# Optimization experiments

Hardware: AMD Instinct MI355X
Metric: run time of the kernel (lower is better)

## Reference

```python
import jax, jax.numpy as jnp
import numpy as np

B, T, D_IN, H, D_OUT, MLP_H = 512, 1024, 64, 256, 64, 256


def setup_inputs() -> dict:
    key = jax.random.key(0)
    ks = jax.random.split(key, 12)
    s_ih = 1.0 / np.sqrt(H)
    return {
        "x": jax.random.normal(ks[0], (B, T, D_IN), dtype=jnp.float32),
        "mask": jax.random.uniform(ks[1], (B, T, 1), dtype=jnp.float32),
        "h0": jax.random.normal(ks[2], (B, H), dtype=jnp.float32),
        "c0": jax.random.normal(ks[3], (B, H), dtype=jnp.float32),
        # LSTMCell params (PyTorch layout: gates in i, f, g, o order)
        "W_ih": jax.random.uniform(ks[4], (4 * H, D_IN), minval=-s_ih, maxval=s_ih, dtype=jnp.float32),
        "W_hh": jax.random.uniform(ks[5], (4 * H, H), minval=-s_ih, maxval=s_ih, dtype=jnp.float32),
        "b_ih": jax.random.uniform(ks[6], (4 * H,), minval=-s_ih, maxval=s_ih, dtype=jnp.float32),
        "b_hh": jax.random.uniform(ks[7], (4 * H,), minval=-s_ih, maxval=s_ih, dtype=jnp.float32),
        # output MLP: Linear(H, MLP_H) -> ReLU -> Linear(MLP_H, D_OUT)
        "W1": jax.random.normal(ks[8], (MLP_H, H), dtype=jnp.float32) * (1.0 / np.sqrt(H)),
        "b1": jnp.zeros((MLP_H,), dtype=jnp.float32),
        "W2": jax.random.normal(ks[9], (D_OUT, MLP_H), dtype=jnp.float32) * (1.0 / np.sqrt(MLP_H)),
        "b2": jnp.zeros((D_OUT,), dtype=jnp.float32),
    }


def _lstm_scan(x, h0, c0, W_ih, W_hh, b_ih, b_hh):
    # precompute input projections for all timesteps: [T, B, 4H]
    x_tb = jnp.swapaxes(x, 0, 1)  # [T, B, D_IN]
    x_proj = jnp.einsum("tbd,gd->tbg", x_tb, W_ih) + b_ih + b_hh

    def step(carry, xp):
        h, c = carry
        gates = xp + h @ W_hh.T  # [B, 4H]
        i, f, g, o = jnp.split(gates, 4, axis=-1)
        i = jax.nn.sigmoid(i)
        f = jax.nn.sigmoid(f)
        g = jnp.tanh(g)
        o = jax.nn.sigmoid(o)
        c = f * c + i * g
        h = o * jnp.tanh(c)
        return (h, c), h

    _, hs = jax.lax.scan(step, (h0, c0), x_proj)  # hs: [T, B, H]
    return jnp.swapaxes(hs, 0, 1)  # [B, T, H]


def reference(x, mask, h0, c0, W_ih, W_hh, b_ih, b_hh, W1, b1, W2, b2):
    hs = _lstm_scan(x, h0, c0, W_ih, W_hh, b_ih, b_hh)  # [B, T, H]
    y = jax.nn.relu(hs @ W1.T + b1) @ W2.T + b2  # [B, T, D_OUT]
    return y * mask
```

## Files before the change

### kernel.cpp

```cpp
#include <hip/hip_runtime.h>
#include <stdint.h>
#include <stddef.h>

#define T_STEPS 1024
#define BATCH   512
#define HID     256
#define DIN     64

typedef __attribute__((ext_vector_type(8))) short short8;
typedef __attribute__((ext_vector_type(4))) short short4v;
typedef __attribute__((ext_vector_type(2))) short short2v;
typedef __attribute__((ext_vector_type(4))) float float4v;

static __device__ __forceinline__ short f2bf(float f) {
  union { float f; unsigned u; } v; v.f = f;
  unsigned r = (v.u + 0x7FFFu + ((v.u >> 16) & 1u)) >> 16;
  return (short)r;
}
static __device__ __forceinline__ float sigm(float x) {
  return 1.0f / (1.0f + __expf(-x));
}
static __device__ __forceinline__ float tanh_f(float x) {
  return 2.0f / (1.0f + __expf(-2.0f * x)) - 1.0f;
}

__global__ __launch_bounds__(512, 2) void lstm_kernel(
    const float* __restrict__ x, const float* __restrict__ h0,
    const float* __restrict__ c0, const float* __restrict__ W_ih,
    const float* __restrict__ W_hh, const float* __restrict__ b_ih,
    const float* __restrict__ b_hh, float* __restrict__ exch,
    uint16_t* __restrict__ hs) {
  const int tid   = threadIdx.x;
  const int blk   = blockIdx.x;
  const int group = blk & 31;
  const int half  = blk >> 5;
  const int b0    = group * 16;
  const int w     = tid >> 6;
  const int lane  = tid & 63;
  const int quad  = lane >> 4;
  const int l16   = lane & 15;
  const int partner = blk ^ 32;

  __shared__ short Alds[16 * 328];
  __shared__ float Glds[16 * 516];

  short8 bw[10][4];
#pragma unroll
  for (int j = 0; j < 10; ++j) {
    int ktA = (j < 4) ? (half * 4 + j) : (j < 8) ? ((1 - half) * 4 + (j - 4)) : j;
#pragma unroll
    for (int nt = 0; nt < 4; ++nt) {
      int n_loc = w * 64 + nt * 16 + l16;
      int gate  = n_loc >> 7;
      int hh    = n_loc & 127;
      int grow  = gate * 256 + half * 128 + hh;
      const float* src = (ktA < 8)
          ? (W_hh + (size_t)grow * 256 + ktA * 32 + quad * 8)
          : (W_ih + (size_t)grow * 64 + (ktA - 8) * 32 + quad * 8);
      short8 bv;
#pragma unroll
      for (int e = 0; e < 8; ++e) bv[e] = f2bf(src[e]);
      bw[j][nt] = bv;
    }
  }

  const int urow = tid >> 5;
  const int hh0  = (tid & 31) * 4;
  const int xc   = (tid & 31) * 2;
  float bias[4][4];
  float c_reg[4];
#pragma unroll
  for (int g = 0; g < 4; ++g) {
    const float* bi = b_ih + g * 256 + half * 128 + hh0;
    const float* bh = b_hh + g * 256 + half * 128 + hh0;
#pragma unroll
    for (int r = 0; r < 4; ++r) bias[g][r] = bi[r] + bh[r];
  }
  {
    const float* c0p = c0 + (size_t)(b0 + urow) * 256 + half * 128 + hh0;
#pragma unroll
    for (int r = 0; r < 4; ++r) c_reg[r] = c0p[r];
  }

  const int widx = urow * 64 + (hh0 >> 1);
  unsigned long long* sbuf[2];
  const unsigned long long* pbuf[2];
#pragma unroll
  for (int bfi = 0; bfi < 2; ++bfi) {
    sbuf[bfi] = (unsigned long long*)(exch + ((size_t)blk * 2 + bfi) * 2048) + widx;
    pbuf[bfi] = (const unsigned long long*)(exch + ((size_t)partner * 2 + bfi) * 2048) + widx;
  }

  {
    int c8 = (tid & 31) * 8;
    const float* hp = h0 + (size_t)(b0 + urow) * 256 + c8;
    short8 hv;
#pragma unroll
    for (int e = 0; e < 8; ++e) hv[e] = f2bf(hp[e]);
    *(short8*)&Alds[urow * 328 + c8] = hv;
    const float* xp = x + ((size_t)(b0 + urow) * T_STEPS + 0) * DIN + xc;
    short2v xv2; xv2[0] = f2bf(xp[0]); xv2[1] = f2bf(xp[1]);
    *(short2v*)&Alds[urow * 328 + 256 + xc] = xv2;
  }
  __syncthreads();

  const int ownbase = half * 128;
  const int pbase   = (1 - half) * 128;

  for (int t = 0; t < T_STEPS; ++t) {
    float4v acc[4] = {{0.f,0.f,0.f,0.f},{0.f,0.f,0.f,0.f},
                      {0.f,0.f,0.f,0.f},{0.f,0.f,0.f,0.f}};
    int tn = (t + 1 < T_STEPS) ? (t + 1) : t;
    const float* xp = x + ((size_t)(b0 + urow) * T_STEPS + tn) * DIN + xc;
    float xa = xp[0], xb = xp[1];

#pragma unroll
    for (int j = 0; j < 4; ++j) {
      short8 a = *(const short8*)&Alds[l16 * 328 + ownbase + j * 32 + quad * 8];
#pragma unroll
      for (int nt = 0; nt < 4; ++nt)
        acc[nt] = __builtin_amdgcn_mfma_f32_16x16x32_bf16(a, bw[j][nt], acc[nt], 0, 0, 0);
    }
#pragma unroll
    for (int j = 8; j < 10; ++j) {
      short8 a = *(const short8*)&Alds[l16 * 328 + 256 + (j - 8) * 32 + quad * 8];
#pragma unroll
      for (int nt = 0; nt < 4; ++nt)
        acc[nt] = __builtin_amdgcn_mfma_f32_16x16x32_bf16(a, bw[j][nt], acc[nt], 0, 0, 0);
    }

    if (t > 0) {
      int buf = (t - 1) & 1;
      unsigned tag = 1u ^ (((unsigned)(t - 1) >> 1) & 1u);
      const unsigned long long* p = pbuf[buf];
      unsigned long long w0, w1;
      int guard = 0;
      for (;;) {
        w0 = __hip_atomic_load(p,     __ATOMIC_RELAXED, __HIP_MEMORY_SCOPE_AGENT);
        w1 = __hip_atomic_load(p + 1, __ATOMIC_RELAXED, __HIP_MEMORY_SCOPE_AGENT);
        bool ok = (((unsigned)w0 & 1u) == tag) & ((((unsigned)(w0 >> 32)) & 1u) == tag) &
                  (((unsigned)w1 & 1u) == tag) & ((((unsigned)(w1 >> 32)) & 1u) == tag);
        if (ok) break;
        if (++guard > 4096) break;
      }
      union { unsigned u; float f; } f0, f1, f2, f3;
      f0.u = (unsigned)w0; f1.u = (unsigned)(w0 >> 32);
      f2.u = (unsigned)w1; f3.u = (unsigned)(w1 >> 32);
      short4v pv4;
      pv4[0] = f2bf(f0.f); pv4[1] = f2bf(f1.f);
      pv4[2] = f2bf(f2.f); pv4[3] = f2bf(f3.f);
      *(short4v*)&Alds[urow * 328 + pbase + hh0] = pv4;
    }
    __syncthreads();

#pragma unroll
    for (int j = 4; j < 8; ++j) {
      short8 a = *(const short8*)&Alds[l16 * 328 + pbase + (j - 4) * 32 + quad * 8];
#pragma unroll
      for (int nt = 0; nt < 4; ++nt)
        acc[nt] = __builtin_amdgcn_mfma_f32_16x16x32_bf16(a, bw[j][nt], acc[nt], 0, 0, 0);
    }
#pragma unroll
    for (int nt = 0; nt < 4; ++nt) {
      int col = w * 64 + nt * 16 + l16;
#pragma unroll
      for (int r = 0; r < 4; ++r)
        Glds[(quad * 4 + r) * 516 + col] = acc[nt][r];
    }
    __syncthreads();

    float4v ip = *(const float4v*)&Glds[urow * 516 + 0   + hh0];
    float4v fp = *(const float4v*)&Glds[urow * 516 + 128 + hh0];
    float4v gp = *(const float4v*)&Glds[urow * 516 + 256 + hh0];
    float4v op = *(const float4v*)&Glds[urow * 516 + 384 + hh0];
    float hf[4];
    short hb[4];
#pragma unroll
    for (int r = 0; r < 4; ++r) {
      float iv = sigm(ip[r] + bias[0][r]);
      float fv = sigm(fp[r] + bias[1][r]);
      float gv = tanh_f(gp[r] + bias[2][r]);
      float ov = sigm(op[r] + bias[3][r]);
      float cv = fv * c_reg[r] + iv * gv;
      c_reg[r] = cv;
      hf[r] = ov * tanh_f(cv);
      hb[r] = f2bf(hf[r]);
    }
    {
      int buf = t & 1;
      unsigned tag = 1u ^ (((unsigned)t >> 1) & 1u);
      union { float f; unsigned u; } u0, u1, u2, u3;
      u0.f = hf[0]; u1.f = hf[1]; u2.f = hf[2]; u3.f = hf[3];
      unsigned long long w0 = (unsigned long long)((u0.u & ~1u) | tag)
                            | ((unsigned long long)((u1.u & ~1u) | tag) << 32);
      unsigned long long w1 = (unsigned long long)((u2.u & ~1u) | tag)
                            | ((unsigned long long)((u3.u & ~1u) | tag) << 32);
      __hip_atomic_store(sbuf[buf],     w0, __ATOMIC_RELAXED, __HIP_MEMORY_SCOPE_AGENT);
      __hip_atomic_store(sbuf[buf] + 1, w1, __ATOMIC_RELAXED, __HIP_MEMORY_SCOPE_AGENT);
    }
    short4v hv4; hv4[0] = hb[0]; hv4[1] = hb[1]; hv4[2] = hb[2]; hv4[3] = hb[3];
    *(short4v*)&Alds[urow * 328 + ownbase + hh0] = hv4;
    *(short4v*)(hs + ((size_t)(b0 + urow) * T_STEPS + t) * HID + ownbase + hh0) = hv4;
    short2v xv2; xv2[0] = f2bf(xa); xv2[1] = f2bf(xb);
    *(short2v*)&Alds[urow * 328 + 256 + xc] = xv2;
    __syncthreads();
  }
}

__global__ void prep_kernel(const float* __restrict__ W1, const float* __restrict__ W2,
                            short* __restrict__ W1b, short* __restrict__ W2b) {
  int i = blockIdx.x * 512 + threadIdx.x;
  if (i < 65536) W1b[i] = f2bf(W1[i]);
  else           W2b[i - 65536] = f2bf(W2[i - 65536]);
}

__global__ __launch_bounds__(512, 2) void mlp_kernel(
    const uint16_t* __restrict__ hs, const short* __restrict__ W1b,
    const float* __restrict__ b1, const short* __restrict__ W2b,
    const float* __restrict__ b2, const float* __restrict__ mask,
    float* __restrict__ y) {
  const int tid   = threadIdx.x;
  const int rows0 = blockIdx.x * 128;
  const int w     = tid >> 6;
  const int lane  = tid & 63;
  const int quad  = lane >> 4;
  const int l16   = lane & 15;

  __shared__ short S[128 * 264];

#pragma unroll
  for (int kk = 0; kk < 8; ++kk) {
    int c   = tid + kk * 512;
    int row = c >> 5;
    int off = (c & 31) * 8;
    *(short8*)&S[row * 264 + off] =
        *(const short8*)(hs + (size_t)(rows0 + row) * HID + off);
  }

  short8 bf1[2][8];
  float  b1v[2];
#pragma unroll
  for (int nt = 0; nt < 2; ++nt) {
    int n = w * 32 + nt * 16 + l16;
    b1v[nt] = b1[n];
#pragma unroll
    for (int kt = 0; kt < 8; ++kt)
      bf1[nt][kt] = *(const short8*)(W1b + (size_t)n * 256 + kt * 32 + quad * 8);
  }
  __syncthreads();

  float4v acc1[2][8];
#pragma unroll
  for (int nt = 0; nt < 2; ++nt)
#pragma unroll
    for (int mt = 0; mt < 8; ++mt) acc1[nt][mt] = (float4v){0.f,0.f,0.f,0.f};
#pragma unroll
  for (int kt = 0; kt < 8; ++kt) {
#pragma unroll
    for (int mt = 0; mt < 8; ++mt) {
      short8 a = *(const short8*)&S[(mt * 16 + l16) * 264 + kt * 32 + quad * 8];
#pragma unroll
      for (int nt = 0; nt < 2; ++nt)
        acc1[nt][mt] = __builtin_amdgcn_mfma_f32_16x16x32_bf16(a, bf1[nt][kt], acc1[nt][mt], 0, 0, 0);
    }
  }
  __syncthreads();

#pragma unroll
  for (int nt = 0; nt < 2; ++nt) {
    int col = w * 32 + nt * 16 + l16;
#pragma unroll
    for (int mt = 0; mt < 8; ++mt)
#pragma unroll
      for (int r = 0; r < 4; ++r) {
        float v = acc1[nt][mt][r] + b1v[nt];
        v = v > 0.f ? v : 0.f;
        S[(mt * 16 + quad * 4 + r) * 264 + col] = f2bf(v);
      }
  }
  __syncthreads();

  const int mt2 = w >> 1;
  short8 a2[8];
#pragma unroll
  for (int kt = 0; kt < 8; ++kt)
    a2[kt] = *(const short8*)(W2b + (size_t)(mt2 * 16 + l16) * 256 + kt * 32 + quad * 8);
  float4v acc2[4] = {{0.f,0.f,0.f,0.f},{0.f,0.f,0.f,0.f},
                     {0.f,0.f,0.f,0.f},{0.f,0.f,0.f,0.f}};
#pragma unroll
  for (int kt = 0; kt < 8; ++kt) {
#pragma unroll
    for (int nt2 = 0; nt2 < 4; ++nt2) {
      int n0 = (w & 1) * 64 + nt2 * 16;
      short8 b = *(const short8*)&S[(n0 + l16) * 264 + kt * 32 + quad * 8];
      acc2[nt2] = __builtin_amdgcn_mfma_f32_16x16x32_bf16(a2[kt], b, acc2[nt2], 0, 0, 0);
    }
  }
  const float* b2p = b2 + mt2 * 16 + quad * 4;
  float b2v0 = b2p[0], b2v1 = b2p[1], b2v2 = b2p[2], b2v3 = b2p[3];
#pragma unroll
  for (int nt2 = 0; nt2 < 4; ++nt2) {
    int R = rows0 + (w & 1) * 64 + nt2 * 16 + l16;
    float m = mask[R];
    float4v out;
    out[0] = (acc2[nt2][0] + b2v0) * m;
    out[1] = (acc2[nt2][1] + b2v1) * m;
    out[2] = (acc2[nt2][2] + b2v2) * m;
    out[3] = (acc2[nt2][3] + b2v3) * m;
    *(float4v*)(y + (size_t)R * 64 + mt2 * 16 + quad * 4) = out;
  }
}

extern "C" void kernel_launch(void* const* d_in, const int* in_sizes, int n_in,
                              void* d_out, int out_size, void* d_ws, size_t ws_size,
                              hipStream_t stream) {
  (void)in_sizes; (void)n_in; (void)out_size; (void)ws_size;
  const float* x    = (const float*)d_in[0];
  const float* mask = (const float*)d_in[1];
  const float* h0   = (const float*)d_in[2];
  const float* c0   = (const float*)d_in[3];
  const float* W_ih = (const float*)d_in[4];
  const float* W_hh = (const float*)d_in[5];
  const float* b_ih = (const float*)d_in[6];
  const float* b_hh = (const float*)d_in[7];
  const float* W1   = (const float*)d_in[8];
  const float* b1   = (const float*)d_in[9];
  const float* W2   = (const float*)d_in[10];
  const float* b2   = (const float*)d_in[11];
  float* y = (float*)d_out;

  char* ws = (char*)d_ws;
  float*    exch = (float*)ws;
  short*    W1b  = (short*)(ws + (1u << 20));
  short*    W2b  = (short*)(ws + (1u << 20) + 131072);
  uint16_t* hs   = (uint16_t*)(ws + (2u << 20));

  prep_kernel<<<160, 512, 0, stream>>>(W1, W2, W1b, W2b);
  lstm_kernel<<<64, 512, 0, stream>>>(x, h0, c0, W_ih, W_hh, b_ih, b_hh, exch, hs);
  mlp_kernel<<<4096, 512, 0, stream>>>(hs, W1b, b1, W2b, b2, mask, y);
}
```

Before: 3.668 ms.

## Add same-XCD fast path for partner hidden-state exchange via sc0 16-byte messages

Each block records its XCC id in a table and checks whether its partner block runs on the same XCD. If it does, the per-step hidden-state exchange uses a single 16-byte sc0 store and load carrying bf16 payload between step-id sentinels. This is meant to poll at L2 rather than device scope, cutting the latency of the serial cross-block handoff at every timestep. The original tagged fp32 exchange is still written every step and serves as the fallback, so store traffic rises and correctness depends on a 16-byte store being seen atomically.

```diff
diff --git a/kernel.cpp b/kernel.cpp
--- a/kernel.cpp
+++ b/kernel.cpp
@@ -11,6 +11,7 @@
 typedef __attribute__((ext_vector_type(4))) short short4v;
 typedef __attribute__((ext_vector_type(2))) short short2v;
 typedef __attribute__((ext_vector_type(4))) float float4v;
+typedef __attribute__((ext_vector_type(4))) unsigned int uint4v;
 
 static __device__ __forceinline__ short f2bf(float f) {
   union { float f; unsigned u; } v; v.f = f;
@@ -22,6 +23,16 @@
 }
 static __device__ __forceinline__ float tanh_f(float x) {
   return 2.0f / (1.0f + __expf(-2.0f * x)) - 1.0f;
+}
+
+static __device__ __forceinline__ void st16_sc0(float* p, uint4v v) {
+  asm volatile("global_store_dwordx4 %0, %1, off sc0" :: "v"(p), "v"(v) : "memory");
+}
+static __device__ __forceinline__ uint4v ld16_sc0(const float* p) {
+  uint4v r;
+  asm volatile("global_load_dwordx4 %0, %1, off sc0\n\ts_waitcnt vmcnt(0)"
+               : "=v"(r) : "v"(p) : "memory");
+  return r;
 }
 
 __global__ __launch_bounds__(512, 2) void lstm_kernel(
@@ -29,6 +40,7 @@
     const float* __restrict__ c0, const float* __restrict__ W_ih,
     const float* __restrict__ W_hh, const float* __restrict__ b_ih,
     const float* __restrict__ b_hh, float* __restrict__ exch,
+    float* __restrict__ exchf, unsigned* __restrict__ tbl,
     uint16_t* __restrict__ hs) {
   const int tid   = threadIdx.x;
   const int blk   = blockIdx.x;
@@ -43,6 +55,45 @@
 
   __shared__ short Alds[16 * 328];
   __shared__ float Glds[16 * 516];
+  __shared__ int s_fastex;
+
+  const int urow = tid >> 5;
+  const int hh0  = (tid & 31) * 4;
+  const int xc   = (tid & 31) * 2;
+
+  const int widx = urow * 64 + (hh0 >> 1);
+  unsigned long long* sbuf[2];
+  const unsigned long long* pbuf[2];
+  float* sfast[2];
+  const float* pfast[2];
+#pragma unroll
+  for (int bfi = 0; bfi < 2; ++bfi) {
+    sbuf[bfi]  = (unsigned long long*)(exch + ((size_t)blk * 2 + bfi) * 2048) + widx;
+    pbuf[bfi]  = (const unsigned long long*)(exch + ((size_t)partner * 2 + bfi) * 2048) + widx;
+    sfast[bfi] = exchf + ((size_t)blk * 2 + bfi) * 2048 + (widx << 1);
+    pfast[bfi] = exchf + ((size_t)partner * 2 + bfi) * 2048 + (widx << 1);
+  }
+
+  {
+    uint4v z; z[0] = 0u; z[1] = 0u; z[2] = 0u; z[3] = 0u;
+    st16_sc0(sfast[0], z);
+    st16_sc0(sfast[1], z);
+  }
+  __syncthreads();
+  if (tid == 0) {
+    int xcd;
+    asm volatile("s_getreg_b32 %0, hwreg(HW_REG_XCC_ID)" : "=s"(xcd));
+    unsigned my = 0x5AB00000u | ((unsigned)xcd & 0xFFu);
+    __hip_atomic_store(&tbl[blk], my, __ATOMIC_RELAXED, __HIP_MEMORY_SCOPE_AGENT);
+    unsigned pv = 0;
+    for (int g2 = 0; g2 < (1 << 16); ++g2) {
+      pv = __hip_atomic_load(&tbl[partner], __ATOMIC_RELAXED, __HIP_MEMORY_SCOPE_AGENT);
+      if ((pv & 0xFFFFFF00u) == 0x5AB00000u) break;
+      __builtin_amdgcn_s_sleep(8);
+    }
+    s_fastex = (((pv & 0xFFFFFF00u) == 0x5AB00000u) &&
+                ((pv & 0xFFu) == (my & 0xFFu))) ? 1 : 0;
+  }
 
   short8 bw[10][4];
 #pragma unroll
@@ -64,9 +115,6 @@
     }
   }
 
-  const int urow = tid >> 5;
-  const int hh0  = (tid & 31) * 4;
-  const int xc   = (tid & 31) * 2;
   float bias[4][4];
   float c_reg[4];
 #pragma unroll
@@ -80,15 +128,6 @@
     const float* c0p = c0 + (size_t)(b0 + urow) * 256 + half * 128 + hh0;
 #pragma unroll
     for (int r = 0; r < 4; ++r) c_reg[r] = c0p[r];
-  }
-
-  const int widx = urow * 64 + (hh0 >> 1);
-  unsigned long long* sbuf[2];
-  const unsigned long long* pbuf[2];
-#pragma unroll
-  for (int bfi = 0; bfi < 2; ++bfi) {
-    sbuf[bfi] = (unsigned long long*)(exch + ((size_t)blk * 2 + bfi) * 2048) + widx;
-    pbuf[bfi] = (const unsigned long long*)(exch + ((size_t)partner * 2 + bfi) * 2048) + widx;
   }
 
   {
@@ -103,6 +142,7 @@
     *(short2v*)&Alds[urow * 328 + 256 + xc] = xv2;
   }
   __syncthreads();
+  const int fastex = s_fastex;
 
   const int ownbase = half * 128;
   const int pbase   = (1 - half) * 128;
@@ -131,24 +171,39 @@
 
     if (t > 0) {
       int buf = (t - 1) & 1;
-      unsigned tag = 1u ^ (((unsigned)(t - 1) >> 1) & 1u);
-      const unsigned long long* p = pbuf[buf];
-      unsigned long long w0, w1;
-      int guard = 0;
-      for (;;) {
-        w0 = __hip_atomic_load(p,     __ATOMIC_RELAXED, __HIP_MEMORY_SCOPE_AGENT);
-        w1 = __hip_atomic_load(p + 1, __ATOMIC_RELAXED, __HIP_MEMORY_SCOPE_AGENT);
-        bool ok = (((unsigned)w0 & 1u) == tag) & ((((unsigned)(w0 >> 32)) & 1u) == tag) &
-                  (((unsigned)w1 & 1u) == tag) & ((((unsigned)(w1 >> 32)) & 1u) == tag);
-        if (ok) break;
-        if (++guard > 4096) break;
+      short4v pv4;
+      bool got = false;
+      if (fastex) {
+        unsigned expect = 0xC0DE0000u + (unsigned)(t - 1);
+        for (int g2 = 0; g2 < 128; ++g2) {
+          uint4v v = ld16_sc0(pfast[buf]);
+          if (v[0] == expect && v[3] == expect) {
+            pv4[0] = (short)(v[1] & 0xFFFFu); pv4[1] = (short)(v[1] >> 16);
+            pv4[2] = (short)(v[2] & 0xFFFFu); pv4[3] = (short)(v[2] >> 16);
+            got = true;
+            break;
+          }
+        }
       }
-      union { unsigned u; float f; } f0, f1, f2, f3;
-      f0.u = (unsigned)w0; f1.u = (unsigned)(w0 >> 32);
-      f2.u = (unsigned)w1; f3.u = (unsigned)(w1 >> 32);
-      short4v pv4;
-      pv4[0] = f2bf(f0.f); pv4[1] = f2bf(f1.f);
-      pv4[2] = f2bf(f2.f); pv4[3] = f2bf(f3.f);
+      if (!got) {
+        unsigned tag = 1u ^ (((unsigned)(t - 1) >> 1) & 1u);
+        const unsigned long long* p = pbuf[buf];
+        unsigned long long w0, w1;
+        int guard = 0;
+        for (;;) {
+          w0 = __hip_atomic_load(p,     __ATOMIC_RELAXED, __HIP_MEMORY_SCOPE_AGENT);
+          w1 = __hip_atomic_load(p + 1, __ATOMIC_RELAXED, __HIP_MEMORY_SCOPE_AGENT);
+          bool ok = (((unsigned)w0 & 1u) == tag) & ((((unsigned)(w0 >> 32)) & 1u) == tag) &
+                    (((unsigned)w1 & 1u) == tag) & ((((unsigned)(w1 >> 32)) & 1u) == tag);
+          if (ok) break;
+          if (++guard > 4096) break;
+        }
+        union { unsigned u; float f; } g0, g1, g2, g3;
+        g0.u = (unsigned)w0; g1.u = (unsigned)(w0 >> 32);
+        g2.u = (unsigned)w1; g3.u = (unsigned)(w1 >> 32);
+        pv4[0] = f2bf(g0.f); pv4[1] = f2bf(g1.f);
+        pv4[2] = f2bf(g2.f); pv4[3] = f2bf(g3.f);
+      }
       *(short4v*)&Alds[urow * 328 + pbase + hh0] = pv4;
     }
     __syncthreads();
@@ -188,6 +243,15 @@
     }
     {
       int buf = t & 1;
+      if (fastex) {
+        unsigned idw = 0xC0DE0000u + (unsigned)t;
+        unsigned pay01 = (unsigned)(unsigned short)hb[0]
+                       | ((unsigned)(unsigned short)hb[1] << 16);
+        unsigned pay23 = (unsigned)(unsigned short)hb[2]
+                       | ((unsigned)(unsigned short)hb[3] << 16);
+        uint4v sv; sv[0] = idw; sv[1] = pay01; sv[2] = pay23; sv[3] = idw;
+        st16_sc0(sfast[buf], sv);
+      }
       unsigned tag = 1u ^ (((unsigned)t >> 1) & 1u);
       union { float f; unsigned u; } u0, u1, u2, u3;
       u0.f = hf[0]; u1.f = hf[1]; u2.f = hf[2]; u3.f = hf[3];
@@ -208,8 +272,11 @@
 }
 
 __global__ void prep_kernel(const float* __restrict__ W1, const float* __restrict__ W2,
-                            short* __restrict__ W1b, short* __restrict__ W2b) {
+                            short* __restrict__ W1b, short* __restrict__ W2b,
+                            unsigned* __restrict__ tbl) {
   int i = blockIdx.x * 512 + threadIdx.x;
+  if (i < 64)
+    __hip_atomic_store(&tbl[i], 0u, __ATOMIC_RELAXED, __HIP_MEMORY_SCOPE_AGENT);
   if (i < 65536) W1b[i] = f2bf(W1[i]);
   else           W2b[i - 65536] = f2bf(W2[i - 65536]);
 }
@@ -330,12 +397,14 @@
   float* y = (float*)d_out;
 
   char* ws = (char*)d_ws;
-  float*    exch = (float*)ws;
-  short*    W1b  = (short*)(ws + (1u << 20));
-  short*    W2b  = (short*)(ws + (1u << 20) + 131072);
-  uint16_t* hs   = (uint16_t*)(ws + (2u << 20));
-
-  prep_kernel<<<160, 512, 0, stream>>>(W1, W2, W1b, W2b);
-  lstm_kernel<<<64, 512, 0, stream>>>(x, h0, c0, W_ih, W_hh, b_ih, b_hh, exch, hs);
+  float*    exch  = (float*)ws;
+  float*    exchf = (float*)(ws + (1u << 20));
+  short*    W1b   = (short*)(ws + (2u << 20));
+  short*    W2b   = (short*)(ws + (2u << 20) + 131072);
+  unsigned* tbl   = (unsigned*)(ws + (2u << 20) + 131072 + 32768);
+  uint16_t* hs    = (uint16_t*)(ws + (3u << 20));
+
+  prep_kernel<<<160, 512, 0, stream>>>(W1, W2, W1b, W2b, tbl);
+  lstm_kernel<<<64, 512, 0, stream>>>(x, h0, c0, W_ih, W_hh, b_ih, b_hh, exch, exchf, tbl, hs);
   mlp_kernel<<<4096, 512, 0, stream>>>(hs, W1b, b1, W2b, b2, mask, y);
 }
```

Measured after the change: 7.724 ms. +110.6%, slower.

## Interleave two batch groups per block to hide partner h-exchange latency

Applied to the files above, without the earlier changes.

Each LSTM block now processes two 16-row batch groups (A and B) using 32 blocks instead of 64. The partner h-exchange for one group overlaps the MFMA work of the other. The gate layout is reorganized so each lane holds all four gates for its hidden unit, which removes the Glds staging buffer and one barrier. Polling now uses non-blocking atomic_add-0 issued early with s_sleep backoff, and the hs global store is deferred by one step. The trade-off is half the blocks and CUs in use, more registers, and more serial work per block.

```diff
diff --git a/kernel.cpp b/kernel.cpp
--- a/kernel.cpp
+++ b/kernel.cpp
@@ -22,6 +22,21 @@
 }
 static __device__ __forceinline__ float tanh_f(float x) {
   return 2.0f / (1.0f + __expf(-2.0f * x)) - 1.0f;
+}
+
+static __device__ __forceinline__ void apoll_issue(const unsigned long long* p,
+                                                   unsigned long long& r0,
+                                                   unsigned long long& r1) {
+  unsigned long long z = 0;
+  asm volatile("global_atomic_add_x2 %0, %2, %3, off sc0\n\t"
+               "global_atomic_add_x2 %1, %2, %3, off offset:8 sc0"
+               : "=&v"(r0), "=&v"(r1)
+               : "v"(p), "v"(z)
+               : "memory");
+}
+static __device__ __forceinline__ void apoll_wait(unsigned long long& r0,
+                                                  unsigned long long& r1) {
+  asm volatile("s_waitcnt vmcnt(0)" : "+v"(r0), "+v"(r1) :: "memory");
 }
 
 __global__ __launch_bounds__(512, 2) void lstm_kernel(
@@ -32,179 +47,251 @@
     uint16_t* __restrict__ hs) {
   const int tid   = threadIdx.x;
   const int blk   = blockIdx.x;
-  const int group = blk & 31;
-  const int half  = blk >> 5;
-  const int b0    = group * 16;
+  const int p     = blk & 15;
+  const int half  = blk >> 4;
+  const int partner = blk ^ 16;
+  const int b0A   = (2 * p) * 16;
+  const int b0B   = (2 * p + 1) * 16;
   const int w     = tid >> 6;
   const int lane  = tid & 63;
   const int quad  = lane >> 4;
   const int l16   = lane & 15;
-  const int partner = blk ^ 32;
-
-  __shared__ short Alds[16 * 328];
-  __shared__ float Glds[16 * 516];
+  const int w16l  = w * 16 + l16;
+
+  __shared__ short AldsA[16 * 328];
+  __shared__ short AldsB[16 * 328];
+
+  const int urow = tid >> 5;
+  const int hh0  = (tid & 31) * 4;
+  const int xc   = (tid & 31) * 2;
+
+  const int widx = tid * 2;
+  unsigned long long* const sb_base =
+      (unsigned long long*)exch + (size_t)blk * 4096 + widx;
+  const unsigned long long* const pb_base =
+      (const unsigned long long*)exch + (size_t)partner * 4096 + widx;
 
   short8 bw[10][4];
 #pragma unroll
   for (int j = 0; j < 10; ++j) {
     int ktA = (j < 4) ? (half * 4 + j) : (j < 8) ? ((1 - half) * 4 + (j - 4)) : j;
 #pragma unroll
-    for (int nt = 0; nt < 4; ++nt) {
-      int n_loc = w * 64 + nt * 16 + l16;
-      int gate  = n_loc >> 7;
-      int hh    = n_loc & 127;
-      int grow  = gate * 256 + half * 128 + hh;
+    for (int g = 0; g < 4; ++g) {
+      int grow = g * 256 + half * 128 + w16l;
       const float* src = (ktA < 8)
           ? (W_hh + (size_t)grow * 256 + ktA * 32 + quad * 8)
           : (W_ih + (size_t)grow * 64 + (ktA - 8) * 32 + quad * 8);
       short8 bv;
 #pragma unroll
       for (int e = 0; e < 8; ++e) bv[e] = f2bf(src[e]);
-      bw[j][nt] = bv;
-    }
-  }
-
-  const int urow = tid >> 5;
-  const int hh0  = (tid & 31) * 4;
-  const int xc   = (tid & 31) * 2;
-  float bias[4][4];
-  float c_reg[4];
-#pragma unroll
-  for (int g = 0; g < 4; ++g) {
-    const float* bi = b_ih + g * 256 + half * 128 + hh0;
-    const float* bh = b_hh + g * 256 + half * 128 + hh0;
-#pragma unroll
-    for (int r = 0; r < 4; ++r) bias[g][r] = bi[r] + bh[r];
-  }
-  {
-    const float* c0p = c0 + (size_t)(b0 + urow) * 256 + half * 128 + hh0;
-#pragma unroll
-    for (int r = 0; r < 4; ++r) c_reg[r] = c0p[r];
-  }
-
-  const int widx = urow * 64 + (hh0 >> 1);
-  unsigned long long* sbuf[2];
-  const unsigned long long* pbuf[2];
-#pragma unroll
-  for (int bfi = 0; bfi < 2; ++bfi) {
-    sbuf[bfi] = (unsigned long long*)(exch + ((size_t)blk * 2 + bfi) * 2048) + widx;
-    pbuf[bfi] = (const unsigned long long*)(exch + ((size_t)partner * 2 + bfi) * 2048) + widx;
+      bw[j][g] = bv;
+    }
+  }
+
+  const int hh_abs = half * 128 + w16l;
+  float bias_g[4];
+#pragma unroll
+  for (int g = 0; g < 4; ++g)
+    bias_g[g] = b_ih[g * 256 + hh_abs] + b_hh[g * 256 + hh_abs];
+  float cA[4], cB[4];
+#pragma unroll
+  for (int r = 0; r < 4; ++r) {
+    cA[r] = c0[(size_t)(b0A + quad * 4 + r) * 256 + hh_abs];
+    cB[r] = c0[(size_t)(b0B + quad * 4 + r) * 256 + hh_abs];
   }
 
   {
     int c8 = (tid & 31) * 8;
-    const float* hp = h0 + (size_t)(b0 + urow) * 256 + c8;
     short8 hv;
-#pragma unroll
-    for (int e = 0; e < 8; ++e) hv[e] = f2bf(hp[e]);
-    *(short8*)&Alds[urow * 328 + c8] = hv;
-    const float* xp = x + ((size_t)(b0 + urow) * T_STEPS + 0) * DIN + xc;
-    short2v xv2; xv2[0] = f2bf(xp[0]); xv2[1] = f2bf(xp[1]);
-    *(short2v*)&Alds[urow * 328 + 256 + xc] = xv2;
+    const float* hpA = h0 + (size_t)(b0A + urow) * 256 + c8;
+#pragma unroll
+    for (int e = 0; e < 8; ++e) hv[e] = f2bf(hpA[e]);
+    *(short8*)&AldsA[urow * 328 + c8] = hv;
+    const float* hpB = h0 + (size_t)(b0B + urow) * 256 + c8;
+#pragma unroll
+    for (int e = 0; e < 8; ++e) hv[e] = f2bf(hpB[e]);
+    *(short8*)&AldsB[urow * 328 + c8] = hv;
+    const float* xpA = x + ((size_t)(b0A + urow) * T_STEPS + 0) * DIN + xc;
+    short2v xv; xv[0] = f2bf(xpA[0]); xv[1] = f2bf(xpA[1]);
+    *(short2v*)&AldsA[urow * 328 + 256 + xc] = xv;
+    const float* xpB = x + ((size_t)(b0B + urow) * T_STEPS + 0) * DIN + xc;
+    xv[0] = f2bf(xpB[0]); xv[1] = f2bf(xpB[1]);
+    *(short2v*)&AldsB[urow * 328 + 256 + xc] = xv;
   }
   __syncthreads();
 
   const int ownbase = half * 128;
   const int pbase   = (1 - half) * 128;
 
+#define PH1(AL, ACC)                                                          \
+  _Pragma("unroll")                                                           \
+  for (int j = 0; j < 4; ++j) {                                               \
+    short8 a = *(const short8*)&AL[l16 * 328 + ownbase + j * 32 + quad * 8];  \
+    _Pragma("unroll")                                                         \
+    for (int g = 0; g < 4; ++g)                                               \
+      ACC[g] = __builtin_amdgcn_mfma_f32_16x16x32_bf16(a, bw[j][g], ACC[g], 0, 0, 0); \
+  }                                                                           \
+  _Pragma("unroll")                                                           \
+  for (int j = 8; j < 10; ++j) {                                              \
+    short8 a = *(const short8*)&AL[l16 * 328 + 256 + (j - 8) * 32 + quad * 8];\
+    _Pragma("unroll")                                                         \
+    for (int g = 0; g < 4; ++g)                                               \
+      ACC[g] = __builtin_amdgcn_mfma_f32_16x16x32_bf16(a, bw[j][g], ACC[g], 0, 0, 0); \
+  }
+
+#define PH2(AL, ACC)                                                          \
+  _Pragma("unroll")                                                           \
+  for (int j = 4; j < 8; ++j) {                                               \
+    short8 a = *(const short8*)&AL[l16 * 328 + pbase + (j - 4) * 32 + quad * 8]; \
+    _Pragma("unroll")                                                         \
+    for (int g = 0; g < 4; ++g)                                               \
+      ACC[g] = __builtin_amdgcn_mfma_f32_16x16x32_bf16(a, bw[j][g], ACC[g], 0, 0, 0); \
+  }
+
+#define CHECK_POLL(PB, R0, R1, PV)                                            \
+  do {                                                                        \
+    unsigned tag2 = (((unsigned)(t - 1) >> 1) & 1u) ? 3u : 1u;                \
+    int guard = 0;                                                            \
+    for (;;) {                                                                \
+      bool ok = ((((unsigned)R0) & 3u) == tag2) &                             \
+                ((((unsigned)(R0 >> 32)) & 3u) == tag2) &                     \
+                ((((unsigned)R1) & 3u) == tag2) &                             \
+                ((((unsigned)(R1 >> 32)) & 3u) == tag2);                      \
+      if (ok) break;                                                          \
+      if (++guard > 4096) break;                                              \
+      __builtin_amdgcn_s_sleep(1);                                            \
+      apoll_issue(PB, R0, R1);                                                \
+      apoll_wait(R0, R1);                                                     \
+    }                                                                         \
+    union { unsigned u; float f; } q0, q1, q2, q3;                            \
+    q0.u = (unsigned)R0; q1.u = (unsigned)(R0 >> 32);                         \
+    q2.u = (unsigned)R1; q3.u = (unsigned)(R1 >> 32);                         \
+    PV[0] = f2bf(q0.f); PV[1] = f2bf(q1.f);                                   \
+    PV[2] = f2bf(q2.f); PV[3] = f2bf(q3.f);                                   \
+  } while (0)
+
+#define UPD(ACC, CREG, HF, HB)                                                \
+  _Pragma("unroll")                                                           \
+  for (int r = 0; r < 4; ++r) {                                               \
+    float iv = sigm(ACC[0][r] + bias_g[0]);                                   \
+    float fv = sigm(ACC[1][r] + bias_g[1]);                                   \
+    float gv = tanh_f(ACC[2][r] + bias_g[2]);                                 \
+    float ov = sigm(ACC[3][r] + bias_g[3]);                                   \
+    float cv = fv * CREG[r] + iv * gv;                                        \
+    CREG[r] = cv;                                                             \
+    HF[r] = ov * tanh_f(cv);                                                  \
+    HB[r] = f2bf(HF[r]);                                                      \
+  }
+
+#define PUB(SB, HF)                                                           \
+  do {                                                                        \
+    unsigned tag2 = (((unsigned)t >> 1) & 1u) ? 3u : 1u;                      \
+    union { float f; unsigned u; } u0, u1, u2, u3;                            \
+    u0.f = HF[0]; u1.f = HF[1]; u2.f = HF[2]; u3.f = HF[3];                   \
+    unsigned long long w0 = (unsigned long long)((u0.u & ~3u) | tag2)         \
+                          | ((unsigned long long)((u1.u & ~3u) | tag2) << 32);\
+    unsigned long long w1 = (unsigned long long)((u2.u & ~3u) | tag2)         \
+                          | ((unsigned long long)((u3.u & ~3u) | tag2) << 32);\
+    __hip_atomic_store(SB,     w0, __ATOMIC_RELAXED, __HIP_MEMORY_SCOPE_AGENT); \
+    __hip_atomic_store(SB + 1, w1, __ATOMIC_RELAXED, __HIP_MEMORY_SCOPE_AGENT); \
+  } while (0)
+
   for (int t = 0; t < T_STEPS; ++t) {
-    float4v acc[4] = {{0.f,0.f,0.f,0.f},{0.f,0.f,0.f,0.f},
-                      {0.f,0.f,0.f,0.f},{0.f,0.f,0.f,0.f}};
+    const unsigned long long* pbA = pb_base + (size_t)(((t - 1) & 1)) * 1024;
+    const unsigned long long* pbB = pb_base + (size_t)(2 + ((t - 1) & 1)) * 1024;
+    unsigned long long* sbA = sb_base + (size_t)(t & 1) * 1024;
+    unsigned long long* sbB = sb_base + (size_t)(2 + (t & 1)) * 1024;
+
+    unsigned long long rA0 = 0, rA1 = 0, rB0 = 0, rB1 = 0;
+    float4v accA[4] = {{0.f,0.f,0.f,0.f},{0.f,0.f,0.f,0.f},
+                       {0.f,0.f,0.f,0.f},{0.f,0.f,0.f,0.f}};
+    float4v accB[4] = {{0.f,0.f,0.f,0.f},{0.f,0.f,0.f,0.f},
+                       {0.f,0.f,0.f,0.f},{0.f,0.f,0.f,0.f}};
+
+    if (t > 0) apoll_issue(pbA, rA0, rA1);
+
     int tn = (t + 1 < T_STEPS) ? (t + 1) : t;
-    const float* xp = x + ((size_t)(b0 + urow) * T_STEPS + tn) * DIN + xc;
-    float xa = xp[0], xb = xp[1];
-
-#pragma unroll
-    for (int j = 0; j < 4; ++j) {
-      short8 a = *(const short8*)&Alds[l16 * 328 + ownbase + j * 32 + quad * 8];
-#pragma unroll
-      for (int nt = 0; nt < 4; ++nt)
-        acc[nt] = __builtin_amdgcn_mfma_f32_16x16x32_bf16(a, bw[j][nt], acc[nt], 0, 0, 0);
-    }
-#pragma unroll
-    for (int j = 8; j < 10; ++j) {
-      short8 a = *(const short8*)&Alds[l16 * 328 + 256 + (j - 8) * 32 + quad * 8];
-#pragma unroll
-      for (int nt = 0; nt < 4; ++nt)
-        acc[nt] = __builtin_amdgcn_mfma_f32_16x16x32_bf16(a, bw[j][nt], acc[nt], 0, 0, 0);
-    }
-
+    const float* xpA = x + ((size_t)(b0A + urow) * T_STEPS + tn) * DIN + xc;
+    float xa0 = xpA[0], xa1 = xpA[1];
+
+    PH1(AldsA, accA);
+
+    if (t > 0) apoll_issue(pbB, rB0, rB1);
+
+    const float* xpB = x + ((size_t)(b0B + urow) * T_STEPS + tn) * DIN + xc;
+    float xb0 = xpB[0], xb1 = xpB[1];
+
+    PH1(AldsB, accB);
+
+    short4v hvA, hvB;
     if (t > 0) {
-      int buf = (t - 1) & 1;
-      unsigned tag = 1u ^ (((unsigned)(t - 1) >> 1) & 1u);
-      const unsigned long long* p = pbuf[buf];
-      unsigned long long w0, w1;
-      int guard = 0;
-      for (;;) {
-        w0 = __hip_atomic_load(p,     __ATOMIC_RELAXED, __HIP_MEMORY_SCOPE_AGENT);
-        w1 = __hip_atomic_load(p + 1, __ATOMIC_RELAXED, __HIP_MEMORY_SCOPE_AGENT);
-        bool ok = (((unsigned)w0 & 1u) == tag) & ((((unsigned)(w0 >> 32)) & 1u) == tag) &
-                  (((unsigned)w1 & 1u) == tag) & ((((unsigned)(w1 >> 32)) & 1u) == tag);
-        if (ok) break;
-        if (++guard > 4096) break;
-      }
-      union { unsigned u; float f; } f0, f1, f2, f3;
-      f0.u = (unsigned)w0; f1.u = (unsigned)(w0 >> 32);
-      f2.u = (unsigned)w1; f3.u = (unsigned)(w1 >> 32);
-      short4v pv4;
-      pv4[0] = f2bf(f0.f); pv4[1] = f2bf(f1.f);
-      pv4[2] = f2bf(f2.f); pv4[3] = f2bf(f3.f);
-      *(short4v*)&Alds[urow * 328 + pbase + hh0] = pv4;
+      hvA = *(const short4v*)&AldsA[urow * 328 + ownbase + hh0];
+      hvB = *(const short4v*)&AldsB[urow * 328 + ownbase + hh0];
+    }
+
+    if (t > 0) {
+      apoll_wait(rA0, rA1);
+      short4v pvA;
+      CHECK_POLL(pbA, rA0, rA1, pvA);
+#pragma unroll
+      for (int r = 0; r < 4; ++r)
+        AldsA[(quad * 4 + r) * 328 + pbase + w16l] = pvA[r];
     }
     __syncthreads();
 
-#pragma unroll
-    for (int j = 4; j < 8; ++j) {
-      short8 a = *(const short8*)&Alds[l16 * 328 + pbase + (j - 4) * 32 + quad * 8];
-#pragma unroll
-      for (int nt = 0; nt < 4; ++nt)
-        acc[nt] = __builtin_amdgcn_mfma_f32_16x16x32_bf16(a, bw[j][nt], acc[nt], 0, 0, 0);
-    }
-#pragma unroll
-    for (int nt = 0; nt < 4; ++nt) {
-      int col = w * 64 + nt * 16 + l16;
+    PH2(AldsA, accA);
+    float hfA[4]; short hbA[4];
+    UPD(accA, cA, hfA, hbA);
+#pragma unroll
+    for (int r = 0; r < 4; ++r)
+      AldsA[(quad * 4 + r) * 328 + ownbase + w16l] = hbA[r];
+    {
+      short2v xv; xv[0] = f2bf(xa0); xv[1] = f2bf(xa1);
+      *(short2v*)&AldsA[urow * 328 + 256 + xc] = xv;
+    }
+
+    if (t > 0) {
+      apoll_wait(rB0, rB1);
+      short4v pvB;
+      CHECK_POLL(pbB, rB0, rB1, pvB);
 #pragma unroll
       for (int r = 0; r < 4; ++r)
-        Glds[(quad * 4 + r) * 516 + col] = acc[nt][r];
+        AldsB[(quad * 4 + r) * 328 + pbase + w16l] = pvB[r];
     }
     __syncthreads();
 
-    float4v ip = *(const float4v*)&Glds[urow * 516 + 0   + hh0];
-    float4v fp = *(const float4v*)&Glds[urow * 516 + 128 + hh0];
-    float4v gp = *(const float4v*)&Glds[urow * 516 + 256 + hh0];
-    float4v op = *(const float4v*)&Glds[urow * 516 + 384 + hh0];
-    float hf[4];
-    short hb[4];
-#pragma unroll
-    for (int r = 0; r < 4; ++r) {
-      float iv = sigm(ip[r] + bias[0][r]);
-      float fv = sigm(fp[r] + bias[1][r]);
-      float gv = tanh_f(gp[r] + bias[2][r]);
-      float ov = sigm(op[r] + bias[3][r]);
-      float cv = fv * c_reg[r] + iv * gv;
-      c_reg[r] = cv;
-      hf[r] = ov * tanh_f(cv);
-      hb[r] = f2bf(hf[r]);
-    }
+    PH2(AldsB, accB);
+    float hfB[4]; short hbB[4];
+    UPD(accB, cB, hfB, hbB);
+#pragma unroll
+    for (int r = 0; r < 4; ++r)
+      AldsB[(quad * 4 + r) * 328 + ownbase + w16l] = hbB[r];
     {
-      int buf = t & 1;
-      unsigned tag = 1u ^ (((unsigned)t >> 1) & 1u);
-      union { float f; unsigned u; } u0, u1, u2, u3;
-      u0.f = hf[0]; u1.f = hf[1]; u2.f = hf[2]; u3.f = hf[3];
-      unsigned long long w0 = (unsigned long long)((u0.u & ~1u) | tag)
-                            | ((unsigned long long)((u1.u & ~1u) | tag) << 32);
-      unsigned long long w1 = (unsigned long long)((u2.u & ~1u) | tag)
-                            | ((unsigned long long)((u3.u & ~1u) | tag) << 32);
-      __hip_atomic_store(sbuf[buf],     w0, __ATOMIC_RELAXED, __HIP_MEMORY_SCOPE_AGENT);
-      __hip_atomic_store(sbuf[buf] + 1, w1, __ATOMIC_RELAXED, __HIP_MEMORY_SCOPE_AGENT);
-    }
-    short4v hv4; hv4[0] = hb[0]; hv4[1] = hb[1]; hv4[2] = hb[2]; hv4[3] = hb[3];
-    *(short4v*)&Alds[urow * 328 + ownbase + hh0] = hv4;
-    *(short4v*)(hs + ((size_t)(b0 + urow) * T_STEPS + t) * HID + ownbase + hh0) = hv4;
-    short2v xv2; xv2[0] = f2bf(xa); xv2[1] = f2bf(xb);
-    *(short2v*)&Alds[urow * 328 + 256 + xc] = xv2;
+      short2v xv; xv[0] = f2bf(xb0); xv[1] = f2bf(xb1);
+      *(short2v*)&AldsB[urow * 328 + 256 + xc] = xv;
+    }
+
+    PUB(sbA, hfA);
+    PUB(sbB, hfB);
+
+    if (t > 0) {
+      *(short4v*)(hs + ((size_t)(b0A + urow) * T_STEPS + (t - 1)) * HID + ownbase + hh0) = hvA;
+      *(short4v*)(hs + ((size_t)(b0B + urow) * T_STEPS + (t - 1)) * HID + ownbase + hh0) = hvB;
+    }
     __syncthreads();
   }
+
+  {
+    short4v hvA = *(const short4v*)&AldsA[urow * 328 + ownbase + hh0];
+    *(short4v*)(hs + ((size_t)(b0A + urow) * T_STEPS + (T_STEPS - 1)) * HID + ownbase + hh0) = hvA;
+    short4v hvB = *(const short4v*)&AldsB[urow * 328 + ownbase + hh0];
+    *(short4v*)(hs + ((size_t)(b0B + urow) * T_STEPS + (T_STEPS - 1)) * HID + ownbase + hh0) = hvB;
+  }
+#undef PH1
+#undef PH2
+#undef CHECK_POLL
+#undef UPD
+#undef PUB
 }
 
 __global__ void prep_kernel(const float* __restrict__ W1, const float* __restrict__ W2,
@@ -336,6 +423,6 @@
   uint16_t* hs   = (uint16_t*)(ws + (2u << 20));
 
   prep_kernel<<<160, 512, 0, stream>>>(W1, W2, W1b, W2b);
-  lstm_kernel<<<64, 512, 0, stream>>>(x, h0, c0, W_ih, W_hh, b_ih, b_hh, exch, hs);
+  lstm_kernel<<<32, 512, 0, stream>>>(x, h0, c0, W_ih, W_hh, b_ih, b_hh, exch, hs);
   mlp_kernel<<<4096, 512, 0, stream>>>(hs, W1b, b1, W2b, b2, mask, y);
 }
```

Result: slower. 6.275 ms (+71.1%).

## Run each batch group's LSTM in one 1024-thread block, dropping cross-block exchange

Applied to the files above, without the earlier changes.

The LSTM recurrence for each 16-row batch group now runs inside a single 1024-thread block (32 blocks) instead of two 512-thread blocks that traded half of h through global memory with atomic spin-waits. Each wave owns 16 hidden units across all four gates, so gate activations come straight from MFMA accumulators with no Glds round-trip. The A buffer is double-buffered so each step needs only one barrier. In exchange, only 32 CUs are used, each wave holds 40 short8 weight fragments in registers, and the hs store for a step is deferred to the next iteration.

```diff
diff --git a/kernel.cpp b/kernel.cpp
--- a/kernel.cpp
+++ b/kernel.cpp
@@ -9,7 +9,6 @@
 
 typedef __attribute__((ext_vector_type(8))) short short8;
 typedef __attribute__((ext_vector_type(4))) short short4v;
-typedef __attribute__((ext_vector_type(2))) short short2v;
 typedef __attribute__((ext_vector_type(4))) float float4v;
 
 static __device__ __forceinline__ short f2bf(float f) {
@@ -24,186 +23,109 @@
   return 2.0f / (1.0f + __expf(-2.0f * x)) - 1.0f;
 }
 
-__global__ __launch_bounds__(512, 2) void lstm_kernel(
+__global__ __launch_bounds__(1024, 4) void lstm_kernel(
     const float* __restrict__ x, const float* __restrict__ h0,
     const float* __restrict__ c0, const float* __restrict__ W_ih,
     const float* __restrict__ W_hh, const float* __restrict__ b_ih,
-    const float* __restrict__ b_hh, float* __restrict__ exch,
-    uint16_t* __restrict__ hs) {
-  const int tid   = threadIdx.x;
-  const int blk   = blockIdx.x;
-  const int group = blk & 31;
-  const int half  = blk >> 5;
-  const int b0    = group * 16;
-  const int w     = tid >> 6;
-  const int lane  = tid & 63;
-  const int quad  = lane >> 4;
-  const int l16   = lane & 15;
-  const int partner = blk ^ 32;
-
-  __shared__ short Alds[16 * 328];
-  __shared__ float Glds[16 * 516];
+    const float* __restrict__ b_hh, uint16_t* __restrict__ hs) {
+  const int tid  = threadIdx.x;
+  const int blk  = blockIdx.x;
+  const int b0   = blk * 16;
+  const int w    = tid >> 6;
+  const int lane = tid & 63;
+  const int quad = lane >> 4;
+  const int l16  = lane & 15;
+  const int w16l = w * 16 + l16;
+  const int urow = tid >> 6;
+
+  __shared__ short Alds[2][16 * 328];
 
   short8 bw[10][4];
 #pragma unroll
   for (int j = 0; j < 10; ++j) {
-    int ktA = (j < 4) ? (half * 4 + j) : (j < 8) ? ((1 - half) * 4 + (j - 4)) : j;
-#pragma unroll
-    for (int nt = 0; nt < 4; ++nt) {
-      int n_loc = w * 64 + nt * 16 + l16;
-      int gate  = n_loc >> 7;
-      int hh    = n_loc & 127;
-      int grow  = gate * 256 + half * 128 + hh;
-      const float* src = (ktA < 8)
-          ? (W_hh + (size_t)grow * 256 + ktA * 32 + quad * 8)
-          : (W_ih + (size_t)grow * 64 + (ktA - 8) * 32 + quad * 8);
+#pragma unroll
+    for (int g = 0; g < 4; ++g) {
+      int grow = g * 256 + w16l;
+      const float* src = (j < 8)
+          ? (W_hh + (size_t)grow * 256 + j * 32 + quad * 8)
+          : (W_ih + (size_t)grow * 64 + (j - 8) * 32 + quad * 8);
       short8 bv;
 #pragma unroll
       for (int e = 0; e < 8; ++e) bv[e] = f2bf(src[e]);
-      bw[j][nt] = bv;
-    }
-  }
-
-  const int urow = tid >> 5;
-  const int hh0  = (tid & 31) * 4;
-  const int xc   = (tid & 31) * 2;
-  float bias[4][4];
+      bw[j][g] = bv;
+    }
+  }
+
+  float bias_g[4];
+#pragma unroll
+  for (int g = 0; g < 4; ++g)
+    bias_g[g] = b_ih[g * 256 + w16l] + b_hh[g * 256 + w16l];
   float c_reg[4];
 #pragma unroll
-  for (int g = 0; g < 4; ++g) {
-    const float* bi = b_ih + g * 256 + half * 128 + hh0;
-    const float* bh = b_hh + g * 256 + half * 128 + hh0;
-#pragma unroll
-    for (int r = 0; r < 4; ++r) bias[g][r] = bi[r] + bh[r];
-  }
+  for (int r = 0; r < 4; ++r)
+    c_reg[r] = c0[(size_t)(b0 + quad * 4 + r) * 256 + w16l];
+
   {
-    const float* c0p = c0 + (size_t)(b0 + urow) * 256 + half * 128 + hh0;
-#pragma unroll
-    for (int r = 0; r < 4; ++r) c_reg[r] = c0p[r];
-  }
-
-  const int widx = urow * 64 + (hh0 >> 1);
-  unsigned long long* sbuf[2];
-  const unsigned long long* pbuf[2];
-#pragma unroll
-  for (int bfi = 0; bfi < 2; ++bfi) {
-    sbuf[bfi] = (unsigned long long*)(exch + ((size_t)blk * 2 + bfi) * 2048) + widx;
-    pbuf[bfi] = (const unsigned long long*)(exch + ((size_t)partner * 2 + bfi) * 2048) + widx;
-  }
-
-  {
-    int c8 = (tid & 31) * 8;
-    const float* hp = h0 + (size_t)(b0 + urow) * 256 + c8;
-    short8 hv;
-#pragma unroll
-    for (int e = 0; e < 8; ++e) hv[e] = f2bf(hp[e]);
-    *(short8*)&Alds[urow * 328 + c8] = hv;
-    const float* xp = x + ((size_t)(b0 + urow) * T_STEPS + 0) * DIN + xc;
-    short2v xv2; xv2[0] = f2bf(xp[0]); xv2[1] = f2bf(xp[1]);
-    *(short2v*)&Alds[urow * 328 + 256 + xc] = xv2;
-  }
-  __syncthreads();
-
-  const int ownbase = half * 128;
-  const int pbase   = (1 - half) * 128;
+    const float* hp = h0 + (size_t)(b0 + urow) * 256 + lane * 4;
+    short4v hv4;
+#pragma unroll
+    for (int e = 0; e < 4; ++e) hv4[e] = f2bf(hp[e]);
+    *(short4v*)&Alds[0][urow * 328 + lane * 4] = hv4;
+    float xv = x[((size_t)(b0 + urow) * T_STEPS + 0) * DIN + lane];
+    Alds[0][urow * 328 + 256 + lane] = f2bf(xv);
+  }
+  __syncthreads();
 
   for (int t = 0; t < T_STEPS; ++t) {
+    short* RD = Alds[t & 1];
+    short* WR = Alds[1 - (t & 1)];
+
+    if (t > 0) {
+      short4v hv = *(const short4v*)&RD[urow * 328 + lane * 4];
+      *(short4v*)(hs + ((size_t)(b0 + urow) * T_STEPS + (t - 1)) * HID + lane * 4) = hv;
+    }
+    int tn = (t + 1 < T_STEPS) ? (t + 1) : t;
+    float xf = x[((size_t)(b0 + urow) * T_STEPS + tn) * DIN + lane];
+
     float4v acc[4] = {{0.f,0.f,0.f,0.f},{0.f,0.f,0.f,0.f},
                       {0.f,0.f,0.f,0.f},{0.f,0.f,0.f,0.f}};
-    int tn = (t + 1 < T_STEPS) ? (t + 1) : t;
-    const float* xp = x + ((size_t)(b0 + urow) * T_STEPS + tn) * DIN + xc;
-    float xa = xp[0], xb = xp[1];
-
-#pragma unroll
-    for (int j = 0; j < 4; ++j) {
-      short8 a = *(const short8*)&Alds[l16 * 328 + ownbase + j * 32 + quad * 8];
-#pragma unroll
-      for (int nt = 0; nt < 4; ++nt)
-        acc[nt] = __builtin_amdgcn_mfma_f32_16x16x32_bf16(a, bw[j][nt], acc[nt], 0, 0, 0);
+#pragma unroll
+    for (int j = 0; j < 8; ++j) {
+      short8 a = *(const short8*)&RD[l16 * 328 + j * 32 + quad * 8];
+#pragma unroll
+      for (int g = 0; g < 4; ++g)
+        acc[g] = __builtin_amdgcn_mfma_f32_16x16x32_bf16(a, bw[j][g], acc[g], 0, 0, 0);
     }
 #pragma unroll
     for (int j = 8; j < 10; ++j) {
-      short8 a = *(const short8*)&Alds[l16 * 328 + 256 + (j - 8) * 32 + quad * 8];
-#pragma unroll
-      for (int nt = 0; nt < 4; ++nt)
-        acc[nt] = __builtin_amdgcn_mfma_f32_16x16x32_bf16(a, bw[j][nt], acc[nt], 0, 0, 0);
-    }
-
-    if (t > 0) {
-      int buf = (t - 1) & 1;
-      unsigned tag = 1u ^ (((unsigned)(t - 1) >> 1) & 1u);
-      const unsigned long long* p = pbuf[buf];
-      unsigned long long w0, w1;
-      int guard = 0;
-      for (;;) {
-        w0 = __hip_atomic_load(p,     __ATOMIC_RELAXED, __HIP_MEMORY_SCOPE_AGENT);
-        w1 = __hip_atomic_load(p + 1, __ATOMIC_RELAXED, __HIP_MEMORY_SCOPE_AGENT);
-        bool ok = (((unsigned)w0 & 1u) == tag) & ((((unsigned)(w0 >> 32)) & 1u) == tag) &
-                  (((unsigned)w1 & 1u) == tag) & ((((unsigned)(w1 >> 32)) & 1u) == tag);
-        if (ok) break;
-        if (++guard > 4096) break;
-      }
-      union { unsigned u; float f; } f0, f1, f2, f3;
-      f0.u = (unsigned)w0; f1.u = (unsigned)(w0 >> 32);
-      f2.u = (unsigned)w1; f3.u = (unsigned)(w1 >> 32);
-      short4v pv4;
-      pv4[0] = f2bf(f0.f); pv4[1] = f2bf(f1.f);
-      pv4[2] = f2bf(f2.f); pv4[3] = f2bf(f3.f);
-      *(short4v*)&Alds[urow * 328 + pbase + hh0] = pv4;
-    }
-    __syncthreads();
-
-#pragma unroll
-    for (int j = 4; j < 8; ++j) {
-      short8 a = *(const short8*)&Alds[l16 * 328 + pbase + (j - 4) * 32 + quad * 8];
-#pragma unroll
-      for (int nt = 0; nt < 4; ++nt)
-        acc[nt] = __builtin_amdgcn_mfma_f32_16x16x32_bf16(a, bw[j][nt], acc[nt], 0, 0, 0);
-    }
-#pragma unroll
-    for (int nt = 0; nt < 4; ++nt) {
-      int col = w * 64 + nt * 16 + l16;
-#pragma unroll
-      for (int r = 0; r < 4; ++r)
-        Glds[(quad * 4 + r) * 516 + col] = acc[nt][r];
-    }
-    __syncthreads();
-
-    float4v ip = *(const float4v*)&Glds[urow * 516 + 0   + hh0];
-    float4v fp = *(const float4v*)&Glds[urow * 516 + 128 + hh0];
-    float4v gp = *(const float4v*)&Glds[urow * 516 + 256 + hh0];
-    float4v op = *(const float4v*)&Glds[urow * 516 + 384 + hh0];
-    float hf[4];
+      short8 a = *(const short8*)&RD[l16 * 328 + 256 + (j - 8) * 32 + quad * 8];
+#pragma unroll
+      for (int g = 0; g < 4; ++g)
+        acc[g] = __builtin_amdgcn_mfma_f32_16x16x32_bf16(a, bw[j][g], acc[g], 0, 0, 0);
+    }
+
     short hb[4];
 #pragma unroll
     for (int r = 0; r < 4; ++r) {
-      float iv = sigm(ip[r] + bias[0][r]);
-      float fv = sigm(fp[r] + bias[1][r]);
-      float gv = tanh_f(gp[r] + bias[2][r]);
-      float ov = sigm(op[r] + bias[3][r]);
+      float iv = sigm(acc[0][r] + bias_g[0]);
+      float fv = sigm(acc[1][r] + bias_g[1]);
+      float gv = tanh_f(acc[2][r] + bias_g[2]);
+      float ov = sigm(acc[3][r] + bias_g[3]);
       float cv = fv * c_reg[r] + iv * gv;
       c_reg[r] = cv;
-      hf[r] = ov * tanh_f(cv);
-      hb[r] = f2bf(hf[r]);
-    }
-    {
-      int buf = t & 1;
-      unsigned tag = 1u ^ (((unsigned)t >> 1) & 1u);
-      union { float f; unsigned u; } u0, u1, u2, u3;
-      u0.f = hf[0]; u1.f = hf[1]; u2.f = hf[2]; u3.f = hf[3];
-      unsigned long long w0 = (unsigned long long)((u0.u & ~1u) | tag)
-                            | ((unsigned long long)((u1.u & ~1u) | tag) << 32);
-      unsigned long long w1 = (unsigned long long)((u2.u & ~1u) | tag)
-                            | ((unsigned long long)((u3.u & ~1u) | tag) << 32);
-      __hip_atomic_store(sbuf[buf],     w0, __ATOMIC_RELAXED, __HIP_MEMORY_SCOPE_AGENT);
-      __hip_atomic_store(sbuf[buf] + 1, w1, __ATOMIC_RELAXED, __HIP_MEMORY_SCOPE_AGENT);
-    }
-    short4v hv4; hv4[0] = hb[0]; hv4[1] = hb[1]; hv4[2] = hb[2]; hv4[3] = hb[3];
-    *(short4v*)&Alds[urow * 328 + ownbase + hh0] = hv4;
-    *(short4v*)(hs + ((size_t)(b0 + urow) * T_STEPS + t) * HID + ownbase + hh0) = hv4;
-    short2v xv2; xv2[0] = f2bf(xa); xv2[1] = f2bf(xb);
-    *(short2v*)&Alds[urow * 328 + 256 + xc] = xv2;
+      hb[r] = f2bf(ov * tanh_f(cv));
+    }
+#pragma unroll
+    for (int r = 0; r < 4; ++r)
+      WR[(quad * 4 + r) * 328 + w16l] = hb[r];
+    WR[urow * 328 + 256 + lane] = f2bf(xf);
+
     __syncthreads();
+  }
+
+  {
+    short4v hv = *(const short4v*)&Alds[T_STEPS & 1][urow * 328 + lane * 4];
+    *(short4v*)(hs + ((size_t)(b0 + urow) * T_STEPS + (T_STEPS - 1)) * HID + lane * 4) = hv;
   }
 }
 
@@ -330,12 +252,11 @@
   float* y = (float*)d_out;
 
   char* ws = (char*)d_ws;
-  float*    exch = (float*)ws;
-  short*    W1b  = (short*)(ws + (1u << 20));
-  short*    W2b  = (short*)(ws + (1u << 20) + 131072);
-  uint16_t* hs   = (uint16_t*)(ws + (2u << 20));
+  short*    W1b = (short*)ws;
+  short*    W2b = (short*)(ws + 131072);
+  uint16_t* hs  = (uint16_t*)(ws + (1u << 20));
 
   prep_kernel<<<160, 512, 0, stream>>>(W1, W2, W1b, W2b);
-  lstm_kernel<<<64, 512, 0, stream>>>(x, h0, c0, W_ih, W_hh, b_ih, b_hh, exch, hs);
+  lstm_kernel<<<32, 1024, 0, stream>>>(x, h0, c0, W_ih, W_hh, b_ih, b_hh, hs);
   mlp_kernel<<<4096, 512, 0, stream>>>(hs, W1b, b1, W2b, b2, mask, y);
 }
```

Result: slower. 12.17 ms (+231.9%).
